# Optimization experiments

Hardware: AMD Instinct MI355X
Metric: run time of the kernel (lower is better)

The kernel has to match this reference:

```python
import jax, jax.numpy as jnp
import numpy as np
from jax import lax

B, C, H, W = 16, 512, 16, 300
K, G = 8, 2          # k_clusters, g_clusters (gvlad)
OUT = 5994           # n speakers
DN = ('NCHW', 'OIHW', 'NCHW')


def setup_inputs() -> dict:
    key = jax.random.key(0)
    ks = jax.random.split(key, 10)
    s = lambda fan: 1.0 / np.sqrt(fan)
    return {
        'x5': jax.random.normal(ks[0], (B, C, H, W), jnp.float32),
        'x4': jnp.zeros((1, 1, 1, 1), jnp.float32),
        'x3': jnp.zeros((1, 1, 1, 1), jnp.float32),
        'x2': jnp.zeros((1, 1, 1, 1), jnp.float32),
        'x1': jnp.zeros((1, 1, 1, 1), jnp.float32),
        'conv_w': jax.random.normal(ks[1], (C, C, 7, 1), jnp.float32) * s(C * 7),
        'conv_b': jnp.zeros((C,), jnp.float32),
        'cc_w': jax.random.normal(ks[2], (K + G, C, 7, 1), jnp.float32) * s(C * 7),
        'cc_b': jnp.zeros((K + G,), jnp.float32),
        'centroids': jax.random.normal(ks[3], (K + G, C), jnp.float32),
        'fc_w': jax.random.normal(ks[4], (C, C * K), jnp.float32) * s(C * K),
        'fc_b': jnp.zeros((C,), jnp.float32),
        'logit_w': jax.random.normal(ks[5], (OUT, C), jnp.float32) * s(C),
    }


def _conv(x, w, b=None):
    y = lax.conv_general_dilated(x, w, (1, 1), 'VALID', dimension_numbers=DN)
    if b is not None:
        y = y + b[None, :, None, None]
    return y


def _forward(x5, conv_w, conv_b, cc_w, cc_b, centroids, fc_w, fc_b, logit_w):
    feats = jnp.maximum(_conv(x5, conv_w, conv_b), 0.0)      # (B,C,H',W) relu conv
    scores = _conv(x5, cc_w, cc_b)                           # (B,K+G,H',W)
    assign = jax.nn.softmax(scores, axis=1)                  # soft cluster assignment
    # VLAD: sum_hw a[b,k,h,w]*(f[b,c,h,w] - cent[k,c]), computed without
    # materializing the (B,K+G,C,H',W) residual tensor (same math, fused form)
    agg = jnp.einsum('bkhw,bchw->bkc', assign, feats)        # (B,K+G,C)
    asum = jnp.sum(assign, axis=(2, 3))                      # (B,K+G)
    cluster_res = agg - asum[:, :, None] * centroids[None]   # (B,K+G,C)
    cluster_res = cluster_res[:, :K, :]                      # gvlad: drop ghost clusters
    norm = jnp.linalg.norm(cluster_res, axis=-1, keepdims=True)
    cluster_l2 = cluster_res / jnp.maximum(norm, 1e-12)
    vlad = cluster_l2.reshape(-1, K * C)                     # (B, K*C)
    emb = jnp.maximum(vlad @ fc_w.T + fc_b, 0.0)             # (B,C)
    logit = emb @ logit_w.T                                  # (B,OUT)
    return emb, logit


def reference(x5, x4, x3, x2, x1, conv_w, conv_b, cc_w, cc_b, centroids,
              fc_w, fc_b, logit_w):
    # x4..x1 are unused by Decoder.forward (only x5 flows through)
    return _forward(x5, conv_w, conv_b, cc_w, cc_b, centroids, fc_w, fc_b, logit_w)
```

## Files before the change

### kernel.cpp

```cpp
#include <hip/hip_runtime.h>
#include <hip/hip_bf16.h>

typedef __attribute__((ext_vector_type(8))) short bf16x8;
typedef __attribute__((ext_vector_type(4))) float f32x4;

__device__ __forceinline__ void async16(const void* g, void* l) {
    __builtin_amdgcn_global_load_lds(
        (const __attribute__((address_space(1))) unsigned int*)g,
        (__attribute__((address_space(3))) unsigned int*)l, 16, 0, 0);
}

__global__ __launch_bounds__(256) void pack_all(const float* __restrict__ x5,
                                                const float* __restrict__ conv_w,
                                                const float* __restrict__ cc_w,
                                                __hip_bfloat16* __restrict__ X3,
                                                __hip_bfloat16* __restrict__ A2f) {
    __shared__ __align__(16) float smem[64 * 65];
    const int f = blockIdx.x;
    if (f < 10240) {
        float(*tile)[65] = (float(*)[65])smem;
        const int ct = f / 1280, r = f % 1280;
        const int wt = r >> 8, bh = r & 255;
        const int b = bh >> 4, h = bh & 15;
        const int w0 = wt * 64, c0 = ct * 64;
        const int lw = (threadIdx.x & 15) * 4;
        const int lc = threadIdx.x >> 4;
#pragma unroll
        for (int i = 0; i < 4; ++i) {
            const int c = lc + i * 16;
            const int w = w0 + lw;
            const float* src = &x5[((size_t)(b * 512 + c0 + c) * 16 + h) * 300 + w];
            float4 v = {0.f, 0.f, 0.f, 0.f};
            if (w + 3 < 300) v = *(const float4*)src;
            else {
                if (w < 300)     v.x = src[0];
                if (w + 1 < 300) v.y = src[1];
                if (w + 2 < 300) v.z = src[2];
            }
            *(float4*)&tile[c][lw] = v;
        }
        __syncthreads();
        const int sc = (threadIdx.x & 15) * 4;
        const int sw0 = threadIdx.x >> 4;
#pragma unroll
        for (int i = 0; i < 4; ++i) {
            const int wl = sw0 + i * 16;
            const int w = w0 + wl;
            if (w < 300) {
                __hip_bfloat16 p[4];
                p[0] = __float2bfloat16(tile[sc + 0][wl]);
                p[1] = __float2bfloat16(tile[sc + 1][wl]);
                p[2] = __float2bfloat16(tile[sc + 2][wl]);
                p[3] = __float2bfloat16(tile[sc + 3][wl]);
                *(uint2*)&X3[(((size_t)(b * 16 + h) * 300 + w)) * 512 + c0 + sc] = *(uint2*)p;
            }
        }
    } else {
        float* w = smem;
        const int co = f - 10240;
        if (co < 522) {
            const float4* src = (co < 512) ? (const float4*)(conv_w + (size_t)co * 3584)
                                           : (const float4*)(cc_w + (size_t)(co - 512) * 3584);
            for (int i = threadIdx.x; i < 896; i += 256) *(float4*)&w[i * 4] = src[i];
        } else {
            for (int i = threadIdx.x; i < 3584; i += 256) w[i] = 0.f;
        }
        __syncthreads();
        const int g = co >> 4, fl = co & 15;
        for (int chunk = threadIdx.x; chunk < 448; chunk += 256) {
            const int kk0 = chunk * 8;
            const int kt = kk0 >> 5, sq = (kk0 >> 3) & 3;
            __hip_bfloat16 p[8];
#pragma unroll
            for (int j = 0; j < 8; ++j) {
                const int k = kk0 + j;
                p[j] = __float2bfloat16(w[(k & 511) * 7 + (k >> 9)]);
            }
            char* dst = (char*)A2f + (((size_t)g * 112 + kt) * 64 + sq * 16 + fl) * 16;
            *(uint4*)dst = *(uint4*)p;
        }
    }
}

__global__ __launch_bounds__(256, 4) void conv_gemm(
    const __hip_bfloat16* __restrict__ A2f, const __hip_bfloat16* __restrict__ X3,
    const float* __restrict__ conv_b,
    __hip_bfloat16* __restrict__ feats, int m_base) {
    __shared__ __align__(16) char lds[16384];
    const int tid = threadIdx.x;
    const int wv = tid >> 6;
    const int lane = tid & 63;

    const int gid = blockIdx.x;
    const int xcd = gid & 7;
    const int j = gid >> 3;
    const int nb = xcd * 48 + (j >> 1);
    const int m0 = (m_base + (j & 1)) * 128;
    const int b = nb / 24;
    const int nt = nb % 24;

    const int row0 = wv * 16 + (lane >> 2);
    const int kseg = (lane & 3) ^ ((lane >> 3) & 3);
    int n0 = nt * 128 + row0;      if (n0 > 2999) n0 = 2999;
    int n1 = nt * 128 + row0 + 64; if (n1 > 2999) n1 = 2999;
    const char* gB0 = (const char*)X3 + ((size_t)((b * 16 + n0 / 300) * 300 + n0 % 300)) * 1024 + (size_t)kseg * 16;
    const char* gB1 = (const char*)X3 + ((size_t)((b * 16 + n1 / 300) * 300 + n1 % 300)) * 1024 + (size_t)kseg * 16;
    char* lB = lds + wv * 1024 + lane * 16;

    const int wm = (wv & 1) * 64;
    const int wn = (wv >> 1) * 64;
    const int fl = lane & 15;
    const int sq = lane >> 4;
    int boff[4];
#pragma unroll
    for (int i = 0; i < 4; ++i) {
        const int swz = (sq ^ ((fl >> 1) & 3)) * 16;
        boff[i] = (wn + i * 16 + fl) * 64 + swz;
    }
    const char* Af = (const char*)A2f;
    const int gb = (m0 >> 4) + ((wv & 1) << 2);

    f32x4 acc[4][4] = {};
    bf16x8 aC[4], aN[4];

#define ISSUE_B(kt, ph)                                                                \
    {                                                                                  \
        const size_t badd = (size_t)((kt) >> 4) * 307200 + (size_t)((kt) & 15) * 64;   \
        async16(gB0 + badd, lB + (ph) * 8192);                                         \
        async16(gB1 + badd, lB + (ph) * 8192 + 4096);                                  \
    }
#define PRE_A(kt, arr)                                                                 \
    {                                                                                  \
        _Pragma("unroll")                                                              \
        for (int mi = 0; mi < 4; ++mi)                                                 \
            arr[mi] = *(const bf16x8*)(Af + (((size_t)(gb + mi) * 112 + (kt)) << 10) + (lane << 4)); \
    }
#define COMPUTE(ph, arr)                                                               \
    {                                                                                  \
        _Pragma("unroll")                                                              \
        for (int ni = 0; ni < 4; ++ni) {                                               \
            const bf16x8 bv = *(const bf16x8*)(lds + (ph) * 8192 + boff[ni]);          \
            _Pragma("unroll")                                                          \
            for (int mi = 0; mi < 4; ++mi)                                             \
                acc[mi][ni] = __builtin_amdgcn_mfma_f32_16x16x32_bf16(arr[mi], bv, acc[mi][ni], 0, 0, 0); \
        }                                                                              \
    }

    ISSUE_B(0, 0);
    PRE_A(0, aC);
    for (int kt = 0; kt < 112; kt += 2) {
        __syncthreads();
        ISSUE_B(kt + 1, 1);
        PRE_A(kt + 1, aN);
        COMPUTE(0, aC);
        __syncthreads();
        if (kt < 110) { ISSUE_B(kt + 2, 0); PRE_A(kt + 2, aC); }
        COMPUTE(1, aN);
    }
#undef ISSUE_B
#undef PRE_A
#undef COMPUTE

    const int quad4 = (lane >> 4) * 4;
#pragma unroll
    for (int ni = 0; ni < 4; ++ni) {
        const int n = nt * 128 + wn + ni * 16 + fl;
        if (n >= 3000) continue;
#pragma unroll
        for (int mi = 0; mi < 4; ++mi) {
            const int cob = m0 + wm + mi * 16 + quad4;
            const f32x4 v = acc[mi][ni];
            __hip_bfloat16 p[4];
#pragma unroll
            for (int r = 0; r < 4; ++r)
                p[r] = __float2bfloat16(fmaxf(v[r] + conv_b[cob + r], 0.f));
            *(uint2*)&feats[((size_t)(b * 3000 + n)) * 512 + cob] = *(uint2*)p;
        }
    }
}

__global__ __launch_bounds__(256) void scores_gemm(
    const __hip_bfloat16* __restrict__ A2f, const __hip_bfloat16* __restrict__ X3,
    const float* __restrict__ cc_b, float* __restrict__ scores) {
    __shared__ __align__(16) char lds[65536];
    const int tid = threadIdx.x;
    const int wv = tid >> 6;
    const int lane = tid & 63;
    const int gid = blockIdx.x;
    const int xcd = gid & 7;
    const int j = gid >> 3;
    const int b = xcd * 2 + (j >= 12 ? 1 : 0);
    const int nt2 = j % 12;

    const int row0 = wv * 16 + (lane >> 2);
    const int kseg = (lane & 3) ^ ((lane >> 3) & 3);
    const char* gB[4];
#pragma unroll
    for (int q = 0; q < 4; ++q) {
        int n = nt2 * 256 + row0 + q * 64;
        if (n > 2999) n = 2999;
        gB[q] = (const char*)X3 + ((size_t)((b * 16 + n / 300) * 300 + n % 300)) * 1024 + (size_t)kseg * 16;
    }
    char* lB = lds + wv * 1024 + lane * 16;

    const int wn = wv * 64;
    const int fl = lane & 15;
    const int sq = lane >> 4;
    int boff[4];
#pragma unroll
    for (int i = 0; i < 4; ++i) {
        const int swz = (sq ^ ((fl >> 1) & 3)) * 16;
        boff[i] = (wn + i * 16 + fl) * 64 + swz;
    }
    const char* Af = (const char*)A2f + (((size_t)32 * 112) << 10) + (lane << 4);

    f32x4 acc[4] = {};
    bf16x8 aC[2], aN[2];

#define S_ISSUE(ktp, ph)                                                               \
    {                                                                                  \
        const int kt0 = (ktp) * 2;                                                     \
        const size_t ba0 = (size_t)(kt0 >> 4) * 307200 + (size_t)(kt0 & 15) * 64;      \
        const size_t ba1 = (size_t)((kt0 + 1) >> 4) * 307200 + (size_t)((kt0 + 1) & 15) * 64; \
        _Pragma("unroll")                                                              \
        for (int q = 0; q < 4; ++q) {                                                  \
            async16(gB[q] + ba0, lB + (ph) * 32768 + q * 4096);                        \
            async16(gB[q] + ba1, lB + (ph) * 32768 + 16384 + q * 4096);                \
        }                                                                              \
    }
#define S_PREA(ktp, arr)                                                               \
    {                                                                                  \
        arr[0] = *(const bf16x8*)(Af + ((size_t)((ktp) * 2) << 10));                   \
        arr[1] = *(const bf16x8*)(Af + ((size_t)((ktp) * 2 + 1) << 10));               \
    }
#define S_COMP(ph, arr)                                                                \
    {                                                                                  \
        _Pragma("unroll")                                                              \
        for (int kk = 0; kk < 2; ++kk) {                                               \
            _Pragma("unroll")                                                          \
            for (int ni = 0; ni < 4; ++ni) {                                           \
                const bf16x8 bv = *(const bf16x8*)(lds + (ph) * 32768 + kk * 16384 + boff[ni]); \
                acc[ni] = __builtin_amdgcn_mfma_f32_16x16x32_bf16(arr[kk], bv, acc[ni], 0, 0, 0); \
            }                                                                          \
        }                                                                              \
    }

    S_ISSUE(0, 0);
    S_PREA(0, aC);
    for (int ktp = 0; ktp < 56; ktp += 2) {
        __syncthreads();
        S_ISSUE(ktp + 1, 1);
        S_PREA(ktp + 1, aN);
        S_COMP(0, aC);
        __syncthreads();
        if (ktp < 54) { S_ISSUE(ktp + 2, 0); S_PREA(ktp + 2, aC); }
        S_COMP(1, aN);
    }
#undef S_ISSUE
#undef S_PREA
#undef S_COMP

#pragma unroll
    for (int ni = 0; ni < 4; ++ni) {
        const int n = nt2 * 256 + wn + ni * 16 + fl;
        if (n >= 3000) continue;
#pragma unroll
        for (int r = 0; r < 4; ++r) {
            const int k = sq * 4 + r;
            if (k < 10)
                scores[(size_t)(b * 10 + k) * 3000 + n] = acc[ni][r] + cc_b[k];
        }
    }
}

__global__ __launch_bounds__(256) void softmax_assign(float* __restrict__ scores,
                                                      float* __restrict__ asum_part,
                                                      float* __restrict__ agg) {
    const int b = blockIdx.x;
    const int chunk = blockIdx.y;
    const int zbase = (b * 12 + chunk) * 512 + threadIdx.x;
    if (zbase < 81920) agg[zbase] = 0.f;
    if (zbase + 256 < 81920) agg[zbase + 256] = 0.f;

    const int hw = chunk * 256 + threadIdx.x;
    const bool valid = hw < 3000;
    float part[10];
    if (valid) {
        float s[10], mx = -1e30f;
#pragma unroll
        for (int k = 0; k < 10; ++k) { s[k] = scores[(size_t)(b * 10 + k) * 3000 + hw]; mx = fmaxf(mx, s[k]); }
        float sum = 0.f;
#pragma unroll
        for (int k = 0; k < 10; ++k) { part[k] = __expf(s[k] - mx); sum += part[k]; }
        const float inv = 1.f / sum;
#pragma unroll
        for (int k = 0; k < 10; ++k) {
            part[k] *= inv;
            scores[(size_t)(b * 10 + k) * 3000 + hw] = part[k];
        }
    } else {
#pragma unroll
        for (int k = 0; k < 10; ++k) part[k] = 0.f;
    }
    __shared__ float red[4][10];
    const int lane = threadIdx.x & 63, w = threadIdx.x >> 6;
#pragma unroll
    for (int k = 0; k < 10; ++k) {
        float v = part[k];
        for (int off = 32; off; off >>= 1) v += __shfl_xor(v, off, 64);
        if (lane == 0) red[w][k] = v;
    }
    __syncthreads();
    if (threadIdx.x < 10)
        asum_part[(chunk * 16 + b) * 10 + threadIdx.x] =
            red[0][threadIdx.x] + red[1][threadIdx.x] + red[2][threadIdx.x] + red[3][threadIdx.x];
}

__global__ __launch_bounds__(256) void agg_kernel(const __hip_bfloat16* __restrict__ feats,
                                                  const float* __restrict__ assign,
                                                  float* __restrict__ agg) {
    const int chunk = blockIdx.x, b = blockIdx.y;
    const int c = threadIdx.x * 2;
    float acc0[10], acc1[10];
#pragma unroll
    for (int k = 0; k < 10; ++k) { acc0[k] = 0.f; acc1[k] = 0.f; }
    const int hw0 = chunk * 75;
    for (int i = 0; i < 75; ++i) {
        const int hw = hw0 + i;
        const __hip_bfloat162 f2 = *(const __hip_bfloat162*)&feats[((size_t)(b * 3000 + hw)) * 512 + c];
        const float f0 = __bfloat162float(f2.x), f1 = __bfloat162float(f2.y);
#pragma unroll
        for (int k = 0; k < 10; ++k) {
            const float a = assign[(size_t)(b * 10 + k) * 3000 + hw];
            acc0[k] += a * f0;
            acc1[k] += a * f1;
        }
    }
#pragma unroll
    for (int k = 0; k < 10; ++k) {
        atomicAdd(&agg[(size_t)(b * 10 + k) * 512 + c], acc0[k]);
        atomicAdd(&agg[(size_t)(b * 10 + k) * 512 + c + 1], acc1[k]);
    }
}

__global__ __launch_bounds__(256) void fc_fused(const float* __restrict__ agg,
                                                const float* __restrict__ asum_part,
                                                const float* __restrict__ centroids,
                                                const float* __restrict__ fc_w,
                                                const float* __restrict__ fc_b,
                                                float* __restrict__ out) {
    __shared__ float res[4096];
    __shared__ float sasum[8];
    __shared__ float red[4][8];
    __shared__ float scale[8];
    const int b = blockIdx.y;
    const int t = threadIdx.x;
    if (t < 8) {
        float s = 0.f;
#pragma unroll
        for (int p = 0; p < 12; ++p) s += asum_part[(p * 16 + b) * 10 + t];
        sasum[t] = s;
    }
    __syncthreads();
    float sq[8];
#pragma unroll
    for (int k = 0; k < 8; ++k) sq[k] = 0.f;
#pragma unroll
    for (int jj = 0; jj < 16; ++jj) {
        const int i = t + jj * 256;
        const int k = jj >> 1;
        const int c = i & 511;
        const float r = agg[(size_t)(b * 10 + k) * 512 + c] - sasum[k] * centroids[k * 512 + c];
        res[i] = r;
        sq[k] += r * r;
    }
    const int lane = t & 63, w = t >> 6;
#pragma unroll
    for (int k = 0; k < 8; ++k) {
        float v = sq[k];
        for (int off = 32; off; off >>= 1) v += __shfl_xor(v, off, 64);
        if (lane == 0) red[w][k] = v;
    }
    __syncthreads();
    if (t < 8) {
        const float nrm = sqrtf(red[0][t] + red[1][t] + red[2][t] + red[3][t]);
        scale[t] = 1.f / fmaxf(nrm, 1e-12f);
    }
    __syncthreads();

    const int col = t >> 3;
    const int ks = t & 7;
    const int co = blockIdx.x * 32 + col;
    const float4* w4 = (const float4*)(fc_w + (size_t)co * 4096);
    float acc = 0.f;
    for (int i = ks; i < 1024; i += 8) {
        const float4 wv = w4[i];
        const float4 rv = *(const float4*)&res[i * 4];
        acc += (rv.x * wv.x + rv.y * wv.y + rv.z * wv.z + rv.w * wv.w) * scale[i >> 7];
    }
    acc += __shfl_down(acc, 4, 8);
    acc += __shfl_down(acc, 2, 8);
    acc += __shfl_down(acc, 1, 8);
    if (ks == 0) out[b * 512 + co] = fmaxf(acc + fc_b[co], 0.f);
}

__global__ __launch_bounds__(256) void logit_kernel(const float* __restrict__ emb,
                                                    const float* __restrict__ logit_w,
                                                    float* __restrict__ out) {
    __shared__ float se[512];
    const int gid = blockIdx.x;
    const int xcd = gid & 7;
    const int j = gid >> 3;
    const int otile = xcd * 3 + (j >> 4);
    const int b = j & 15;
    se[threadIdx.x] = emb[b * 512 + threadIdx.x];
    se[threadIdx.x + 256] = emb[b * 512 + threadIdx.x + 256];
    __syncthreads();
    const int o = otile * 256 + threadIdx.x;
    if (o < 5994) {
        const float4* w4 = (const float4*)(logit_w + (size_t)o * 512);
        float acc = 0.f;
        for (int i = 0; i < 128; ++i) {
            const float4 w = w4[i];
            acc += w.x * se[4 * i] + w.y * se[4 * i + 1] + w.z * se[4 * i + 2] + w.w * se[4 * i + 3];
        }
        out[8192 + b * 5994 + o] = acc;
    }
}

extern "C" void kernel_launch(void* const* d_in, const int* in_sizes, int n_in,
                              void* d_out, int out_size, void* d_ws, size_t ws_size,
                              hipStream_t stream) {
    (void)in_sizes; (void)n_in; (void)out_size; (void)ws_size;
    const float* x5       = (const float*)d_in[0];
    const float* conv_w   = (const float*)d_in[5];
    const float* conv_b   = (const float*)d_in[6];
    const float* cc_w     = (const float*)d_in[7];
    const float* cc_b     = (const float*)d_in[8];
    const float* centroids= (const float*)d_in[9];
    const float* fc_w     = (const float*)d_in[10];
    const float* fc_b     = (const float*)d_in[11];
    const float* logit_w  = (const float*)d_in[12];
    float* out = (float*)d_out;

    char* ws = (char*)d_ws;
    __hip_bfloat16* X3    = (__hip_bfloat16*)(ws);
    __hip_bfloat16* A2f   = (__hip_bfloat16*)(ws + 78643200);
    __hip_bfloat16* feats = (__hip_bfloat16*)(ws + 83230720);
    float* scores         = (float*)(ws + 132382720);
    float* asum_part      = (float*)(ws + 134302720);
    float* agg            = (float*)(ws + 134310400);

    pack_all<<<dim3(10880), 256, 0, stream>>>(x5, conv_w, cc_w, X3, A2f);
    scores_gemm<<<dim3(192), 256, 0, stream>>>(A2f, X3, cc_b, scores);
    softmax_assign<<<dim3(16, 12), 256, 0, stream>>>(scores, asum_part, agg);
    conv_gemm<<<dim3(768), 256, 0, stream>>>(A2f, X3, conv_b, feats, 0);
    conv_gemm<<<dim3(768), 256, 0, stream>>>(A2f, X3, conv_b, feats, 2);
    agg_kernel<<<dim3(40, 16), 256, 0, stream>>>(feats, scores, agg);
    fc_fused<<<dim3(16, 16), 256, 0, stream>>>(agg, asum_part, centroids, fc_w, fc_b, out);
    logit_kernel<<<dim3(384), 256, 0, stream>>>(out, logit_w, out);
}
```

Baseline: 653.1 us.

## Fuse softmax into scores GEMM and VLAD aggregation into conv GEMM epilogue

Folds the softmax over cluster scores into the scores GEMM epilogue using cross-lane shuffles, and computes the assignment-weighted feature aggregation directly inside the conv GEMM epilogue with atomics. This removes the bf16 feats tensor (about 49MB written and re-read) and two kernel launches, and merges the two half conv launches into one grid. The pack kernel also writes 16-byte instead of 8-byte stores. The cost is a heavier epilogue with many shuffles and atomics per block, plus the conv GEMM now depends on the assign buffer.

```diff
diff --git a/kernel.cpp b/kernel.cpp
--- a/kernel.cpp
+++ b/kernel.cpp
@@ -40,19 +40,17 @@
             *(float4*)&tile[c][lw] = v;
         }
         __syncthreads();
-        const int sc = (threadIdx.x & 15) * 4;
-        const int sw0 = threadIdx.x >> 4;
-#pragma unroll
-        for (int i = 0; i < 4; ++i) {
-            const int wl = sw0 + i * 16;
+        const int sc = (threadIdx.x & 7) * 8;
+        const int sw0 = threadIdx.x >> 3;
+#pragma unroll
+        for (int i = 0; i < 2; ++i) {
+            const int wl = sw0 + i * 32;
             const int w = w0 + wl;
             if (w < 300) {
-                __hip_bfloat16 p[4];
-                p[0] = __float2bfloat16(tile[sc + 0][wl]);
-                p[1] = __float2bfloat16(tile[sc + 1][wl]);
-                p[2] = __float2bfloat16(tile[sc + 2][wl]);
-                p[3] = __float2bfloat16(tile[sc + 3][wl]);
-                *(uint2*)&X3[(((size_t)(b * 16 + h) * 300 + w)) * 512 + c0 + sc] = *(uint2*)p;
+                __hip_bfloat16 p[8];
+#pragma unroll
+                for (int j = 0; j < 8; ++j) p[j] = __float2bfloat16(tile[sc + j][wl]);
+                *(uint4*)&X3[(((size_t)(b * 16 + h) * 300 + w)) * 512 + c0 + sc] = *(uint4*)p;
             }
         }
     } else {
@@ -82,107 +80,12 @@
     }
 }
 
-__global__ __launch_bounds__(256, 4) void conv_gemm(
-    const __hip_bfloat16* __restrict__ A2f, const __hip_bfloat16* __restrict__ X3,
-    const float* __restrict__ conv_b,
-    __hip_bfloat16* __restrict__ feats, int m_base) {
-    __shared__ __align__(16) char lds[16384];
-    const int tid = threadIdx.x;
-    const int wv = tid >> 6;
-    const int lane = tid & 63;
-
-    const int gid = blockIdx.x;
-    const int xcd = gid & 7;
-    const int j = gid >> 3;
-    const int nb = xcd * 48 + (j >> 1);
-    const int m0 = (m_base + (j & 1)) * 128;
-    const int b = nb / 24;
-    const int nt = nb % 24;
-
-    const int row0 = wv * 16 + (lane >> 2);
-    const int kseg = (lane & 3) ^ ((lane >> 3) & 3);
-    int n0 = nt * 128 + row0;      if (n0 > 2999) n0 = 2999;
-    int n1 = nt * 128 + row0 + 64; if (n1 > 2999) n1 = 2999;
-    const char* gB0 = (const char*)X3 + ((size_t)((b * 16 + n0 / 300) * 300 + n0 % 300)) * 1024 + (size_t)kseg * 16;
-    const char* gB1 = (const char*)X3 + ((size_t)((b * 16 + n1 / 300) * 300 + n1 % 300)) * 1024 + (size_t)kseg * 16;
-    char* lB = lds + wv * 1024 + lane * 16;
-
-    const int wm = (wv & 1) * 64;
-    const int wn = (wv >> 1) * 64;
-    const int fl = lane & 15;
-    const int sq = lane >> 4;
-    int boff[4];
-#pragma unroll
-    for (int i = 0; i < 4; ++i) {
-        const int swz = (sq ^ ((fl >> 1) & 3)) * 16;
-        boff[i] = (wn + i * 16 + fl) * 64 + swz;
-    }
-    const char* Af = (const char*)A2f;
-    const int gb = (m0 >> 4) + ((wv & 1) << 2);
-
-    f32x4 acc[4][4] = {};
-    bf16x8 aC[4], aN[4];
-
-#define ISSUE_B(kt, ph)                                                                \
-    {                                                                                  \
-        const size_t badd = (size_t)((kt) >> 4) * 307200 + (size_t)((kt) & 15) * 64;   \
-        async16(gB0 + badd, lB + (ph) * 8192);                                         \
-        async16(gB1 + badd, lB + (ph) * 8192 + 4096);                                  \
-    }
-#define PRE_A(kt, arr)                                                                 \
-    {                                                                                  \
-        _Pragma("unroll")                                                              \
-        for (int mi = 0; mi < 4; ++mi)                                                 \
-            arr[mi] = *(const bf16x8*)(Af + (((size_t)(gb + mi) * 112 + (kt)) << 10) + (lane << 4)); \
-    }
-#define COMPUTE(ph, arr)                                                               \
-    {                                                                                  \
-        _Pragma("unroll")                                                              \
-        for (int ni = 0; ni < 4; ++ni) {                                               \
-            const bf16x8 bv = *(const bf16x8*)(lds + (ph) * 8192 + boff[ni]);          \
-            _Pragma("unroll")                                                          \
-            for (int mi = 0; mi < 4; ++mi)                                             \
-                acc[mi][ni] = __builtin_amdgcn_mfma_f32_16x16x32_bf16(arr[mi], bv, acc[mi][ni], 0, 0, 0); \
-        }                                                                              \
-    }
-
-    ISSUE_B(0, 0);
-    PRE_A(0, aC);
-    for (int kt = 0; kt < 112; kt += 2) {
-        __syncthreads();
-        ISSUE_B(kt + 1, 1);
-        PRE_A(kt + 1, aN);
-        COMPUTE(0, aC);
-        __syncthreads();
-        if (kt < 110) { ISSUE_B(kt + 2, 0); PRE_A(kt + 2, aC); }
-        COMPUTE(1, aN);
-    }
-#undef ISSUE_B
-#undef PRE_A
-#undef COMPUTE
-
-    const int quad4 = (lane >> 4) * 4;
-#pragma unroll
-    for (int ni = 0; ni < 4; ++ni) {
-        const int n = nt * 128 + wn + ni * 16 + fl;
-        if (n >= 3000) continue;
-#pragma unroll
-        for (int mi = 0; mi < 4; ++mi) {
-            const int cob = m0 + wm + mi * 16 + quad4;
-            const f32x4 v = acc[mi][ni];
-            __hip_bfloat16 p[4];
-#pragma unroll
-            for (int r = 0; r < 4; ++r)
-                p[r] = __float2bfloat16(fmaxf(v[r] + conv_b[cob + r], 0.f));
-            *(uint2*)&feats[((size_t)(b * 3000 + n)) * 512 + cob] = *(uint2*)p;
-        }
-    }
-}
-
 __global__ __launch_bounds__(256) void scores_gemm(
     const __hip_bfloat16* __restrict__ A2f, const __hip_bfloat16* __restrict__ X3,
-    const float* __restrict__ cc_b, float* __restrict__ scores) {
+    const float* __restrict__ cc_b, float* __restrict__ assign,
+    float* __restrict__ asum_part, float* __restrict__ agg) {
     __shared__ __align__(16) char lds[65536];
+    __shared__ float sred[4][4][4];
     const int tid = threadIdx.x;
     const int wv = tid >> 6;
     const int lane = tid & 63;
@@ -192,6 +95,14 @@
     const int b = xcd * 2 + (j >= 12 ? 1 : 0);
     const int nt2 = j % 12;
 
+    {
+        const int base = gid * 427;
+        for (int i = tid; i < 427; i += 256) {
+            const int idx = base + i;
+            if (idx < 81920) agg[idx] = 0.f;
+        }
+    }
+
     const int row0 = wv * 16 + (lane >> 2);
     const int kseg = (lane & 3) ^ ((lane >> 3) & 3);
     const char* gB[4];
@@ -260,86 +171,176 @@
 #undef S_PREA
 #undef S_COMP
 
+    float pa[4] = {0.f, 0.f, 0.f, 0.f};
 #pragma unroll
     for (int ni = 0; ni < 4; ++ni) {
         const int n = nt2 * 256 + wn + ni * 16 + fl;
-        if (n >= 3000) continue;
+        const bool nval = (n < 3000);
+        float s[4];
 #pragma unroll
         for (int r = 0; r < 4; ++r) {
             const int k = sq * 4 + r;
-            if (k < 10)
-                scores[(size_t)(b * 10 + k) * 3000 + n] = acc[ni][r] + cc_b[k];
-        }
-    }
-}
-
-__global__ __launch_bounds__(256) void softmax_assign(float* __restrict__ scores,
-                                                      float* __restrict__ asum_part,
-                                                      float* __restrict__ agg) {
-    const int b = blockIdx.x;
-    const int chunk = blockIdx.y;
-    const int zbase = (b * 12 + chunk) * 512 + threadIdx.x;
-    if (zbase < 81920) agg[zbase] = 0.f;
-    if (zbase + 256 < 81920) agg[zbase + 256] = 0.f;
-
-    const int hw = chunk * 256 + threadIdx.x;
-    const bool valid = hw < 3000;
-    float part[10];
-    if (valid) {
-        float s[10], mx = -1e30f;
-#pragma unroll
-        for (int k = 0; k < 10; ++k) { s[k] = scores[(size_t)(b * 10 + k) * 3000 + hw]; mx = fmaxf(mx, s[k]); }
-        float sum = 0.f;
-#pragma unroll
-        for (int k = 0; k < 10; ++k) { part[k] = __expf(s[k] - mx); sum += part[k]; }
-        const float inv = 1.f / sum;
-#pragma unroll
-        for (int k = 0; k < 10; ++k) {
-            part[k] *= inv;
-            scores[(size_t)(b * 10 + k) * 3000 + hw] = part[k];
-        }
-    } else {
-#pragma unroll
-        for (int k = 0; k < 10; ++k) part[k] = 0.f;
-    }
-    __shared__ float red[4][10];
-    const int lane = threadIdx.x & 63, w = threadIdx.x >> 6;
-#pragma unroll
+            s[r] = (k < 10) ? (acc[ni][r] + cc_b[k]) : -1e30f;
+        }
+        float mx = fmaxf(fmaxf(s[0], s[1]), fmaxf(s[2], s[3]));
+        mx = fmaxf(mx, __shfl_xor(mx, 16, 64));
+        mx = fmaxf(mx, __shfl_xor(mx, 32, 64));
+        float e[4], es = 0.f;
+#pragma unroll
+        for (int r = 0; r < 4; ++r) {
+            e[r] = (sq * 4 + r < 10) ? __expf(s[r] - mx) : 0.f;
+            es += e[r];
+        }
+        es += __shfl_xor(es, 16, 64);
+        es += __shfl_xor(es, 32, 64);
+        const float inv = 1.f / es;
+#pragma unroll
+        for (int r = 0; r < 4; ++r) {
+            const int k = sq * 4 + r;
+            const float a = e[r] * inv;
+            if (nval) {
+                if (k < 10) assign[(size_t)(b * 10 + k) * 3000 + n] = a;
+                pa[r] += a;
+            }
+        }
+    }
+#pragma unroll
+    for (int off = 1; off < 16; off <<= 1)
+#pragma unroll
+        for (int r = 0; r < 4; ++r) pa[r] += __shfl_xor(pa[r], off, 64);
+    if (fl == 0) {
+#pragma unroll
+        for (int r = 0; r < 4; ++r) sred[wv][sq][r] = pa[r];
+    }
+    __syncthreads();
+    if (tid < 10)
+        asum_part[(nt2 * 16 + b) * 10 + tid] =
+            sred[0][tid >> 2][tid & 3] + sred[1][tid >> 2][tid & 3] +
+            sred[2][tid >> 2][tid & 3] + sred[3][tid >> 2][tid & 3];
+}
+
+__global__ __launch_bounds__(256, 4) void conv_gemm(
+    const __hip_bfloat16* __restrict__ A2f, const __hip_bfloat16* __restrict__ X3,
+    const float* __restrict__ conv_b, const float* __restrict__ assign,
+    float* __restrict__ agg) {
+    __shared__ __align__(16) char lds[16384];
+    const int tid = threadIdx.x;
+    const int wv = tid >> 6;
+    const int lane = tid & 63;
+
+    const int gid = blockIdx.x;
+    const int xcd = gid & 7;
+    const int j = gid >> 3;
+    const int nb = xcd * 48 + (j >> 2);
+    const int m0 = (j & 3) * 128;
+    const int b = nb / 24;
+    const int nt = nb % 24;
+
+    const int row0 = wv * 16 + (lane >> 2);
+    const int kseg = (lane & 3) ^ ((lane >> 3) & 3);
+    int n0 = nt * 128 + row0;      if (n0 > 2999) n0 = 2999;
+    int n1 = nt * 128 + row0 + 64; if (n1 > 2999) n1 = 2999;
+    const char* gB0 = (const char*)X3 + ((size_t)((b * 16 + n0 / 300) * 300 + n0 % 300)) * 1024 + (size_t)kseg * 16;
+    const char* gB1 = (const char*)X3 + ((size_t)((b * 16 + n1 / 300) * 300 + n1 % 300)) * 1024 + (size_t)kseg * 16;
+    char* lB = lds + wv * 1024 + lane * 16;
+
+    const int wm = (wv & 1) * 64;
+    const int wn = (wv >> 1) * 64;
+    const int fl = lane & 15;
+    const int sq = lane >> 4;
+    int boff[4];
+#pragma unroll
+    for (int i = 0; i < 4; ++i) {
+        const int swz = (sq ^ ((fl >> 1) & 3)) * 16;
+        boff[i] = (wn + i * 16 + fl) * 64 + swz;
+    }
+    const char* Af = (const char*)A2f;
+    const int gb = (m0 >> 4) + ((wv & 1) << 2);
+
+    f32x4 acc[4][4] = {};
+    bf16x8 aC[4], aN[4];
+
+#define ISSUE_B(kt, ph)                                                                \
+    {                                                                                  \
+        const size_t badd = (size_t)((kt) >> 4) * 307200 + (size_t)((kt) & 15) * 64;   \
+        async16(gB0 + badd, lB + (ph) * 8192);                                         \
+        async16(gB1 + badd, lB + (ph) * 8192 + 4096);                                  \
+    }
+#define PRE_A(kt, arr)                                                                 \
+    {                                                                                  \
+        _Pragma("unroll")                                                              \
+        for (int mi = 0; mi < 4; ++mi)                                                 \
+            arr[mi] = *(const bf16x8*)(Af + (((size_t)(gb + mi) * 112 + (kt)) << 10) + (lane << 4)); \
+    }
+#define COMPUTE(ph, arr)                                                               \
+    {                                                                                  \
+        _Pragma("unroll")                                                              \
+        for (int ni = 0; ni < 4; ++ni) {                                               \
+            const bf16x8 bv = *(const bf16x8*)(lds + (ph) * 8192 + boff[ni]);          \
+            _Pragma("unroll")                                                          \
+            for (int mi = 0; mi < 4; ++mi)                                             \
+                acc[mi][ni] = __builtin_amdgcn_mfma_f32_16x16x32_bf16(arr[mi], bv, acc[mi][ni], 0, 0, 0); \
+        }                                                                              \
+    }
+
+    ISSUE_B(0, 0);
+    PRE_A(0, aC);
+    for (int kt = 0; kt < 112; kt += 2) {
+        __syncthreads();
+        ISSUE_B(kt + 1, 1);
+        PRE_A(kt + 1, aN);
+        COMPUTE(0, aC);
+        __syncthreads();
+        if (kt < 110) { ISSUE_B(kt + 2, 0); PRE_A(kt + 2, aC); }
+        COMPUTE(1, aN);
+    }
+#undef ISSUE_B
+#undef PRE_A
+#undef COMPUTE
+
+    const int quad4 = sq * 4;
+#pragma unroll
+    for (int mi = 0; mi < 4; ++mi) {
+        const int cob = m0 + wm + mi * 16 + quad4;
+        const float b0 = conv_b[cob + 0], b1 = conv_b[cob + 1],
+                    b2 = conv_b[cob + 2], b3 = conv_b[cob + 3];
+#pragma unroll
+        for (int ni = 0; ni < 4; ++ni) {
+            acc[mi][ni][0] = fmaxf(acc[mi][ni][0] + b0, 0.f);
+            acc[mi][ni][1] = fmaxf(acc[mi][ni][1] + b1, 0.f);
+            acc[mi][ni][2] = fmaxf(acc[mi][ni][2] + b2, 0.f);
+            acc[mi][ni][3] = fmaxf(acc[mi][ni][3] + b3, 0.f);
+        }
+    }
+    int nn[4];
+#pragma unroll
+    for (int ni = 0; ni < 4; ++ni) nn[ni] = nt * 128 + wn + ni * 16 + fl;
+    const float* asg = assign + (size_t)b * 30000;
     for (int k = 0; k < 10; ++k) {
-        float v = part[k];
-        for (int off = 32; off; off >>= 1) v += __shfl_xor(v, off, 64);
-        if (lane == 0) red[w][k] = v;
-    }
-    __syncthreads();
-    if (threadIdx.x < 10)
-        asum_part[(chunk * 16 + b) * 10 + threadIdx.x] =
-            red[0][threadIdx.x] + red[1][threadIdx.x] + red[2][threadIdx.x] + red[3][threadIdx.x];
-}
-
-__global__ __launch_bounds__(256) void agg_kernel(const __hip_bfloat16* __restrict__ feats,
-                                                  const float* __restrict__ assign,
-                                                  float* __restrict__ agg) {
-    const int chunk = blockIdx.x, b = blockIdx.y;
-    const int c = threadIdx.x * 2;
-    float acc0[10], acc1[10];
-#pragma unroll
-    for (int k = 0; k < 10; ++k) { acc0[k] = 0.f; acc1[k] = 0.f; }
-    const int hw0 = chunk * 75;
-    for (int i = 0; i < 75; ++i) {
-        const int hw = hw0 + i;
-        const __hip_bfloat162 f2 = *(const __hip_bfloat162*)&feats[((size_t)(b * 3000 + hw)) * 512 + c];
-        const float f0 = __bfloat162float(f2.x), f1 = __bfloat162float(f2.y);
-#pragma unroll
-        for (int k = 0; k < 10; ++k) {
-            const float a = assign[(size_t)(b * 10 + k) * 3000 + hw];
-            acc0[k] += a * f0;
-            acc1[k] += a * f1;
-        }
-    }
-#pragma unroll
-    for (int k = 0; k < 10; ++k) {
-        atomicAdd(&agg[(size_t)(b * 10 + k) * 512 + c], acc0[k]);
-        atomicAdd(&agg[(size_t)(b * 10 + k) * 512 + c + 1], acc1[k]);
+        float av[4];
+#pragma unroll
+        for (int ni = 0; ni < 4; ++ni)
+            av[ni] = (nn[ni] < 3000) ? asg[(size_t)k * 3000 + nn[ni]] : 0.f;
+        float part[16];
+#pragma unroll
+        for (int mi = 0; mi < 4; ++mi)
+#pragma unroll
+            for (int r = 0; r < 4; ++r)
+                part[mi * 4 + r] = av[0] * acc[mi][0][r] + av[1] * acc[mi][1][r]
+                                 + av[2] * acc[mi][2][r] + av[3] * acc[mi][3][r];
+#pragma unroll
+        for (int off = 1; off < 16; off <<= 1)
+#pragma unroll
+            for (int i = 0; i < 16; ++i)
+                part[i] += __shfl_xor(part[i], off, 64);
+        if (fl == 0) {
+            float* ag = agg + (size_t)(b * 10 + k) * 512;
+#pragma unroll
+            for (int mi = 0; mi < 4; ++mi)
+#pragma unroll
+                for (int r = 0; r < 4; ++r)
+                    atomicAdd(&ag[m0 + wm + mi * 16 + quad4 + r], part[mi * 4 + r]);
+        }
     }
 }
 
@@ -444,19 +445,15 @@
     float* out = (float*)d_out;
 
     char* ws = (char*)d_ws;
-    __hip_bfloat16* X3    = (__hip_bfloat16*)(ws);
-    __hip_bfloat16* A2f   = (__hip_bfloat16*)(ws + 78643200);
-    __hip_bfloat16* feats = (__hip_bfloat16*)(ws + 83230720);
-    float* scores         = (float*)(ws + 132382720);
-    float* asum_part      = (float*)(ws + 134302720);
-    float* agg            = (float*)(ws + 134310400);
+    __hip_bfloat16* X3  = (__hip_bfloat16*)(ws);
+    __hip_bfloat16* A2f = (__hip_bfloat16*)(ws + 78643200);
+    float* assign       = (float*)(ws + 83230720);
+    float* asum_part    = (float*)(ws + 85150720);
+    float* agg          = (float*)(ws + 85158400);
 
     pack_all<<<dim3(10880), 256, 0, stream>>>(x5, conv_w, cc_w, X3, A2f);
-    scores_gemm<<<dim3(192), 256, 0, stream>>>(A2f, X3, cc_b, scores);
-    softmax_assign<<<dim3(16, 12), 256, 0, stream>>>(scores, asum_part, agg);
-    conv_gemm<<<dim3(768), 256, 0, stream>>>(A2f, X3, conv_b, feats, 0);
-    conv_gemm<<<dim3(768), 256, 0, stream>>>(A2f, X3, conv_b, feats, 2);
-    agg_kernel<<<dim3(40, 16), 256, 0, stream>>>(feats, scores, agg);
+    scores_gemm<<<dim3(192), 256, 0, stream>>>(A2f, X3, cc_b, assign, asum_part, agg);
+    conv_gemm<<<dim3(1536), 256, 0, stream>>>(A2f, X3, conv_b, assign, agg);
     fc_fused<<<dim3(16, 16), 256, 0, stream>>>(agg, asum_part, centroids, fc_w, fc_b, out);
     logit_kernel<<<dim3(384), 256, 0, stream>>>(out, logit_w, out);
 }
```

New measurement: 652.2 us. About the same (-0.1%).
